# Kernel optimization log

Hardware: AMD Instinct MI355X
Metric: run time of the kernel (lower is better)

Reference implementation:

```python
import jax, jax.numpy as jnp
import numpy as np


def setup_inputs() -> dict:
    key = jax.random.key(0)
    k1, k2, k3, k4 = jax.random.split(key, 4)
    T, E, H, I = 256, 16, 2048, 1024
    x = jax.random.normal(k1, (T, H), dtype=jnp.float32)
    router_logits = jax.random.normal(k2, (T, E), dtype=jnp.float32)
    # dequantized GGUF expert weights (math after dequant is plain fp GEMM)
    w1 = jax.random.normal(k3, (E, 2 * I, H), dtype=jnp.float32) * 0.02  # gate/up fused
    w2 = jax.random.normal(k4, (E, H, I), dtype=jnp.float32) * 0.02     # down proj
    return {"x": x, "router_logits": router_logits, "w1": w1, "w2": w2, "top_k": 4}


def reference(x, router_logits, w1, w2, top_k):
    # Router: softmax -> top-k -> renormalize (vLLM fused_moe default)
    probs = jax.nn.softmax(router_logits, axis=-1)            # [T, E]
    topk_vals, topk_idx = jax.lax.top_k(probs, top_k)          # [T, k]
    topk_vals = topk_vals / jnp.sum(topk_vals, axis=-1, keepdims=True)
    T, E = router_logits.shape
    # dense routing weights (zero for non-selected experts)
    route_w = jnp.zeros((T, E), dtype=x.dtype).at[
        jnp.arange(T)[:, None], topk_idx].set(topk_vals)       # [T, E]

    I = w1.shape[1] // 2
    # gate_up projection for all experts: [T, E, 2I]
    h = jnp.einsum('th,eih->tei', x, w1)
    gate, up = h[..., :I], h[..., I:]
    act = jax.nn.silu(gate) * up                               # silu_and_mul [T, E, I]
    # down projection: [T, E, H]
    y = jnp.einsum('tei,ehi->teh', act, w2)
    # combine with routing weights
    out = jnp.einsum('te,teh->th', route_w, y)                 # [T, H]
    return out
```

## Files before the change

kernel.cpp:

```cpp
#include <hip/hip_runtime.h>


typedef __attribute__((ext_vector_type(8))) short bf16x8;
typedef __attribute__((ext_vector_type(4))) float floatx4;

#define T_TOK 256
#define N_EXP 16
#define H_DIM 2048
#define I_DIM 1024
#define MAX_SLOTS 256

__device__ __forceinline__ short f2bf(float f) {
    union { float f; unsigned u; } v; v.f = f;
    unsigned r = (v.u + 0x7FFFu + ((v.u >> 16) & 1u)) >> 16;
    return (short)r;
}
__device__ __forceinline__ float bf2f(short s) {
    union { unsigned u; float f; } v; v.u = ((unsigned)(unsigned short)s) << 16;
    return v.f;
}
__device__ __forceinline__ bf16x8 pack2f4(float4 a, float4 b) {
    bf16x8 r;
    r[0] = f2bf(a.x); r[1] = f2bf(a.y); r[2] = f2bf(a.z); r[3] = f2bf(a.w);
    r[4] = f2bf(b.x); r[5] = f2bf(b.y); r[6] = f2bf(b.z); r[7] = f2bf(b.w);
    return r;
}
__device__ __forceinline__ bf16x8 pack8(const float* __restrict__ p) {
    return pack2f4(*(const float4*)p, *(const float4*)(p + 4));
}

__global__ __launch_bounds__(256) void convert_x_kernel(
    const float* __restrict__ xf, short* __restrict__ xb)
{
    const int i = (blockIdx.x * 256 + threadIdx.x) * 8;
    *(bf16x8*)(xb + i) = pack8(xf + i);
}

__global__ __launch_bounds__(256) void route_kernel(
    const float* __restrict__ logits,
    const int* __restrict__ topk_ptr,
    int* __restrict__ counts, int* __restrict__ tokens,
    int* __restrict__ tok_e, int* __restrict__ tok_slot, float* __restrict__ tok_wt)
{
    __shared__ int lds_counts[N_EXP];
    const int t = threadIdx.x;
    if (t < N_EXP) lds_counts[t] = 0;
    __syncthreads();

    int K = topk_ptr[0];
    if (K > 8) K = 8;
    if (K < 1) K = 1;

    float l[N_EXP];
    #pragma unroll
    for (int j = 0; j < N_EXP; ++j) l[j] = logits[t * N_EXP + j];

    float M = l[0];
    #pragma unroll
    for (int j = 1; j < N_EXP; ++j) M = fmaxf(M, l[j]);

    int idx[8]; float lv[8]; unsigned used = 0u;
    for (int k = 0; k < K; ++k) {
        int bi = 0; float bv = -1e30f;
        #pragma unroll
        for (int j = 0; j < N_EXP; ++j)
            if (!((used >> j) & 1u) && l[j] > bv) { bv = l[j]; bi = j; }
        used |= 1u << bi;
        idx[k] = bi; lv[k] = bv;
    }
    float w[8], s = 0.f;
    for (int k = 0; k < K; ++k) { w[k] = __expf(lv[k] - M); s += w[k]; }
    const float inv = 1.0f / s;

    for (int k = 0; k < K; ++k) {
        const int e = idx[k];
        const int slot = atomicAdd(&lds_counts[e], 1);
        tokens[e * MAX_SLOTS + slot] = t;
        tok_e[t * 8 + k] = e; tok_slot[t * 8 + k] = slot; tok_wt[t * 8 + k] = w[k] * inv;
    }
    __syncthreads();
    if (t < N_EXP) counts[t] = lds_counts[t];
}

template<int MT>
__device__ __forceinline__ void g1_ms(
    int ms, int count, const int* __restrict__ toks, const short* __restrict__ xb,
    const float* __restrict__ wg, const float* __restrict__ wu,
    int quad, int nl, int lane, int iw, int kh, int i_base, int e,
    short* __restrict__ act, floatx4* red)
{
    const short* xr[MT];
    #pragma unroll
    for (int mt = 0; mt < MT; ++mt) {
        int s = ms + mt * 16 + nl;
        if (s >= count) s = count - 1;
        xr[mt] = xb + (size_t)toks[s] * H_DIM + kh * (H_DIM / 2);
    }
    floatx4 ag[MT], au[MT];
    #pragma unroll
    for (int mt = 0; mt < MT; ++mt) { ag[mt] = (floatx4)0.0f; au[mt] = (floatx4)0.0f; }

    for (int k = 0; k < H_DIM / 2; k += 32) {
        const int ko = k + quad * 8;
        float4 g0 = *(const float4*)(wg + ko), g1 = *(const float4*)(wg + ko + 4);
        float4 u0 = *(const float4*)(wu + ko), u1 = *(const float4*)(wu + ko + 4);
        bf16x8 av[MT];
        #pragma unroll
        for (int mt = 0; mt < MT; ++mt) av[mt] = *(const bf16x8*)(xr[mt] + ko);
        bf16x8 bg = pack2f4(g0, g1);
        bf16x8 bu = pack2f4(u0, u1);
        #pragma unroll
        for (int mt = 0; mt < MT; ++mt) {
            ag[mt] = __builtin_amdgcn_mfma_f32_16x16x32_bf16(av[mt], bg, ag[mt], 0, 0, 0);
            au[mt] = __builtin_amdgcn_mfma_f32_16x16x32_bf16(av[mt], bu, au[mt], 0, 0, 0);
        }
    }
    if (kh) {
        #pragma unroll
        for (int mt = 0; mt < MT; ++mt) {
            red[(((iw * 8 + mt) * 2 + 0) * 64) + lane] = ag[mt];
            red[(((iw * 8 + mt) * 2 + 1) * 64) + lane] = au[mt];
        }
    }
    __syncthreads();
    if (!kh) {
        #pragma unroll
        for (int mt = 0; mt < MT; ++mt) {
            floatx4 g = ag[mt] + red[(((iw * 8 + mt) * 2 + 0) * 64) + lane];
            floatx4 u = au[mt] + red[(((iw * 8 + mt) * 2 + 1) * 64) + lane];
            #pragma unroll
            for (int r = 0; r < 4; ++r) {
                const int slot = ms + mt * 16 + quad * 4 + r;
                if (slot < count) {
                    const float gv = g[r], uv = u[r];
                    const float a = gv / (1.0f + __expf(-gv)) * uv;
                    act[(size_t)(e * MAX_SLOTS + slot) * I_DIM + i_base + nl] = f2bf(a);
                }
            }
        }
    }
    __syncthreads();
}

__global__ __launch_bounds__(512, 2) void gemm1_kernel(
    const short* __restrict__ xb,
    const float* __restrict__ w1,
    const int* __restrict__ counts, const int* __restrict__ tokens,
    short* __restrict__ act)
{
    __shared__ floatx4 red[4 * 8 * 2 * 64];
    const int e = blockIdx.x;
    const int count = counts[e];
    if (count == 0) return;
    const int tid = (int)threadIdx.x;
    const int wave = tid >> 6, lane = tid & 63;
    const int iw = wave & 3, kh = wave >> 2;
    const int nl = lane & 15, quad = lane >> 4;
    const int i_base = blockIdx.y * 64 + iw * 16;

    const float* wg = w1 + ((size_t)e * H_DIM + (i_base + nl)) * H_DIM + kh * (H_DIM / 2);
    const float* wu = w1 + ((size_t)e * H_DIM + (I_DIM + i_base + nl)) * H_DIM + kh * (H_DIM / 2);
    const int* toks = tokens + e * MAX_SLOTS;

    for (int ms = 0; ms < count; ms += 128) {
        const int rem = count - ms;
        const int nmt = rem >= 128 ? 8 : ((rem + 15) >> 4);
        switch (nmt) {
            case 1: g1_ms<1>(ms, count, toks, xb, wg, wu, quad, nl, lane, iw, kh, i_base, e, act, red); break;
            case 2: g1_ms<2>(ms, count, toks, xb, wg, wu, quad, nl, lane, iw, kh, i_base, e, act, red); break;
            case 3: g1_ms<3>(ms, count, toks, xb, wg, wu, quad, nl, lane, iw, kh, i_base, e, act, red); break;
            case 4: g1_ms<4>(ms, count, toks, xb, wg, wu, quad, nl, lane, iw, kh, i_base, e, act, red); break;
            case 5: g1_ms<5>(ms, count, toks, xb, wg, wu, quad, nl, lane, iw, kh, i_base, e, act, red); break;
            case 6: g1_ms<6>(ms, count, toks, xb, wg, wu, quad, nl, lane, iw, kh, i_base, e, act, red); break;
            case 7: g1_ms<7>(ms, count, toks, xb, wg, wu, quad, nl, lane, iw, kh, i_base, e, act, red); break;
            default: g1_ms<8>(ms, count, toks, xb, wg, wu, quad, nl, lane, iw, kh, i_base, e, act, red); break;
        }
    }
}

template<int MT>
__device__ __forceinline__ void g2_ms(
    int ms, int count, const short* __restrict__ acte,
    const float* __restrict__ wr,
    int quad, int nl, int lane, int iw, int kh, int h_base, int e,
    short* __restrict__ y, floatx4* red)
{
    const short* ar[MT];
    #pragma unroll
    for (int mt = 0; mt < MT; ++mt) {
        int s = ms + mt * 16 + nl;
        if (s >= count) s = count - 1;
        ar[mt] = acte + (size_t)s * I_DIM + kh * (I_DIM / 2);
    }
    floatx4 acc[MT];
    #pragma unroll
    for (int mt = 0; mt < MT; ++mt) acc[mt] = (floatx4)0.0f;

    for (int k = 0; k < I_DIM / 2; k += 32) {
        const int ko = k + quad * 8;
        float4 b0 = *(const float4*)(wr + ko), b1 = *(const float4*)(wr + ko + 4);
        bf16x8 av[MT];
        #pragma unroll
        for (int mt = 0; mt < MT; ++mt) av[mt] = *(const bf16x8*)(ar[mt] + ko);
        bf16x8 b = pack2f4(b0, b1);
        #pragma unroll
        for (int mt = 0; mt < MT; ++mt)
            acc[mt] = __builtin_amdgcn_mfma_f32_16x16x32_bf16(av[mt], b, acc[mt], 0, 0, 0);
    }
    if (kh) {
        #pragma unroll
        for (int mt = 0; mt < MT; ++mt) red[(iw * 8 + mt) * 64 + lane] = acc[mt];
    }
    __syncthreads();
    if (!kh) {
        #pragma unroll
        for (int mt = 0; mt < MT; ++mt) {
            floatx4 a = acc[mt] + red[(iw * 8 + mt) * 64 + lane];
            #pragma unroll
            for (int r = 0; r < 4; ++r) {
                const int slot = ms + mt * 16 + quad * 4 + r;
                if (slot < count)
                    y[(size_t)(e * MAX_SLOTS + slot) * H_DIM + h_base + nl] = f2bf(a[r]);
            }
        }
    }
    __syncthreads();
}

__global__ __launch_bounds__(512, 4) void gemm2_kernel(
    const short* __restrict__ act,
    const float* __restrict__ w2,
    const int* __restrict__ counts,
    short* __restrict__ y)
{
    __shared__ floatx4 red[4 * 8 * 64];
    const int e = blockIdx.x;
    const int count = counts[e];
    if (count == 0) return;
    const int tid = (int)threadIdx.x;
    const int wave = tid >> 6, lane = tid & 63;
    const int iw = wave & 3, kh = wave >> 2;
    const int nl = lane & 15, quad = lane >> 4;
    const int h_base = blockIdx.y * 64 + iw * 16;

    const float* wr = w2 + ((size_t)e * H_DIM + h_base + nl) * I_DIM + kh * (I_DIM / 2);
    const short* acte = act + (size_t)e * MAX_SLOTS * I_DIM;

    for (int ms = 0; ms < count; ms += 128) {
        const int rem = count - ms;
        const int nmt = rem >= 128 ? 8 : ((rem + 15) >> 4);
        switch (nmt) {
            case 1: g2_ms<1>(ms, count, acte, wr, quad, nl, lane, iw, kh, h_base, e, y, red); break;
            case 2: g2_ms<2>(ms, count, acte, wr, quad, nl, lane, iw, kh, h_base, e, y, red); break;
            case 3: g2_ms<3>(ms, count, acte, wr, quad, nl, lane, iw, kh, h_base, e, y, red); break;
            case 4: g2_ms<4>(ms, count, acte, wr, quad, nl, lane, iw, kh, h_base, e, y, red); break;
            case 5: g2_ms<5>(ms, count, acte, wr, quad, nl, lane, iw, kh, h_base, e, y, red); break;
            case 6: g2_ms<6>(ms, count, acte, wr, quad, nl, lane, iw, kh, h_base, e, y, red); break;
            case 7: g2_ms<7>(ms, count, acte, wr, quad, nl, lane, iw, kh, h_base, e, y, red); break;
            default: g2_ms<8>(ms, count, acte, wr, quad, nl, lane, iw, kh, h_base, e, y, red); break;
        }
    }
}

__global__ __launch_bounds__(256) void gather_kernel(
    const short* __restrict__ y, const int* __restrict__ topk_ptr,
    const int* __restrict__ tok_e, const int* __restrict__ tok_slot,
    const float* __restrict__ tok_wt, float* __restrict__ out)
{
    const int t = blockIdx.x;
    int K = topk_ptr[0];
    if (K > 8) K = 8;
    if (K < 1) K = 1;
    int e[8], sl[8]; float w[8];
    for (int k = 0; k < K; ++k) {
        e[k] = tok_e[t * 8 + k]; sl[k] = tok_slot[t * 8 + k]; w[k] = tok_wt[t * 8 + k];
    }
    for (int h = threadIdx.x; h < H_DIM; h += 256) {
        float s = 0.f;
        for (int k = 0; k < K; ++k)
            s += w[k] * bf2f(y[(size_t)(e[k] * MAX_SLOTS + sl[k]) * H_DIM + h]);
        out[(size_t)t * H_DIM + h] = s;
    }
}

extern "C" void kernel_launch(void* const* d_in, const int* in_sizes, int n_in,
                              void* d_out, int out_size, void* d_ws, size_t ws_size,
                              hipStream_t stream)
{
    const float* x  = (const float*)d_in[0];
    const float* rl = (const float*)d_in[1];
    const float* w1 = (const float*)d_in[2];
    const float* w2 = (const float*)d_in[3];
    const int* topk = (const int*)d_in[4];

    char* ws = (char*)d_ws;
    int*   counts   = (int*)  (ws + 0);
    int*   tokens   = (int*)  (ws + 256);
    int*   tok_e    = (int*)  (ws + 16640);
    int*   tok_slot = (int*)  (ws + 24832);
    float* tok_wt   = (float*)(ws + 33024);
    short* xb       = (short*)(ws + 65536);
    short* act      = (short*)(ws + 1114112);
    short* yb       = (short*)(ws + 9502720);

    convert_x_kernel<<<256, 256, 0, stream>>>(x, xb);
    route_kernel<<<1, 256, 0, stream>>>(rl, topk, counts, tokens, tok_e, tok_slot, tok_wt);
    gemm1_kernel<<<dim3(N_EXP, 16), 512, 0, stream>>>(xb, w1, counts, tokens, act);
    gemm2_kernel<<<dim3(N_EXP, 32), 512, 0, stream>>>(act, w2, counts, yb);
    gather_kernel<<<T_TOK, 256, 0, stream>>>(yb, topk, tok_e, tok_slot, tok_wt, (float*)d_out);
}
```

Baseline: 527.4 us.

## Split GEMM K into four wave slices, shrink blocks, prefetch weights

Both expert GEMM kernels change from 512-thread blocks (4 N-tiles by 2 K-halves) to 256-thread blocks, each covering one 16-column tile with the K dimension split into four wave slices. A three-way LDS reduction combines the partial sums. The grid grows fourfold, which puts more independent blocks on the many CUs of a memory-bound fp32 weight stream. Each wave also software-prefetches the next fp32 weight chunk into registers before the MFMAs. Pointer arithmetic now uses 32-bit offsets. The cost is more LDS reduction traffic, and each block now re-reads the activation rows that its four tiles previously shared.

```diff
diff --git a/kernel.cpp b/kernel.cpp
--- a/kernel.cpp
+++ b/kernel.cpp
@@ -9,6 +9,8 @@
 #define H_DIM 2048
 #define I_DIM 1024
 #define MAX_SLOTS 256
+#define KQ1 (H_DIM / 4)
+#define KQ2 (I_DIM / 4)
 
 __device__ __forceinline__ short f2bf(float f) {
     union { float f; unsigned u; } v; v.f = f;
@@ -86,27 +88,33 @@
 __device__ __forceinline__ void g1_ms(
     int ms, int count, const int* __restrict__ toks, const short* __restrict__ xb,
     const float* __restrict__ wg, const float* __restrict__ wu,
-    int quad, int nl, int lane, int iw, int kh, int i_base, int e,
+    int quad, int nl, int lane, int kq, int i_base, int e,
     short* __restrict__ act, floatx4* red)
 {
-    const short* xr[MT];
+    int xoff[MT];
     #pragma unroll
     for (int mt = 0; mt < MT; ++mt) {
         int s = ms + mt * 16 + nl;
         if (s >= count) s = count - 1;
-        xr[mt] = xb + (size_t)toks[s] * H_DIM + kh * (H_DIM / 2);
+        xoff[mt] = toks[s] * H_DIM + kq * KQ1;
     }
     floatx4 ag[MT], au[MT];
     #pragma unroll
     for (int mt = 0; mt < MT; ++mt) { ag[mt] = (floatx4)0.0f; au[mt] = (floatx4)0.0f; }
 
-    for (int k = 0; k < H_DIM / 2; k += 32) {
-        const int ko = k + quad * 8;
-        float4 g0 = *(const float4*)(wg + ko), g1 = *(const float4*)(wg + ko + 4);
-        float4 u0 = *(const float4*)(wu + ko), u1 = *(const float4*)(wu + ko + 4);
+    const int koff = quad * 8;
+    float4 g0 = *(const float4*)(wg + koff), g1 = *(const float4*)(wg + koff + 4);
+    float4 u0 = *(const float4*)(wu + koff), u1 = *(const float4*)(wu + koff + 4);
+
+    for (int k = 0; k < KQ1; k += 32) {
+        const int nk = (k + 32 < KQ1) ? (k + 32) : k;
+        float4 ng0 = *(const float4*)(wg + nk + koff);
+        float4 ng1 = *(const float4*)(wg + nk + koff + 4);
+        float4 nu0 = *(const float4*)(wu + nk + koff);
+        float4 nu1 = *(const float4*)(wu + nk + koff + 4);
         bf16x8 av[MT];
         #pragma unroll
-        for (int mt = 0; mt < MT; ++mt) av[mt] = *(const bf16x8*)(xr[mt] + ko);
+        for (int mt = 0; mt < MT; ++mt) av[mt] = *(const bf16x8*)(xb + xoff[mt] + k + koff);
         bf16x8 bg = pack2f4(g0, g1);
         bf16x8 bu = pack2f4(u0, u1);
         #pragma unroll
@@ -114,20 +122,25 @@
             ag[mt] = __builtin_amdgcn_mfma_f32_16x16x32_bf16(av[mt], bg, ag[mt], 0, 0, 0);
             au[mt] = __builtin_amdgcn_mfma_f32_16x16x32_bf16(av[mt], bu, au[mt], 0, 0, 0);
         }
-    }
-    if (kh) {
+        g0 = ng0; g1 = ng1; u0 = nu0; u1 = nu1;
+    }
+    if (kq) {
         #pragma unroll
         for (int mt = 0; mt < MT; ++mt) {
-            red[(((iw * 8 + mt) * 2 + 0) * 64) + lane] = ag[mt];
-            red[(((iw * 8 + mt) * 2 + 1) * 64) + lane] = au[mt];
-        }
-    }
-    __syncthreads();
-    if (!kh) {
+            red[(((kq - 1) * 8 + mt) * 2 + 0) * 64 + lane] = ag[mt];
+            red[(((kq - 1) * 8 + mt) * 2 + 1) * 64 + lane] = au[mt];
+        }
+    }
+    __syncthreads();
+    if (kq == 0) {
         #pragma unroll
         for (int mt = 0; mt < MT; ++mt) {
-            floatx4 g = ag[mt] + red[(((iw * 8 + mt) * 2 + 0) * 64) + lane];
-            floatx4 u = au[mt] + red[(((iw * 8 + mt) * 2 + 1) * 64) + lane];
+            floatx4 g = ag[mt], u = au[mt];
+            #pragma unroll
+            for (int q = 0; q < 3; ++q) {
+                g += red[((q * 8 + mt) * 2 + 0) * 64 + lane];
+                u += red[((q * 8 + mt) * 2 + 1) * 64 + lane];
+            }
             #pragma unroll
             for (int r = 0; r < 4; ++r) {
                 const int slot = ms + mt * 16 + quad * 4 + r;
@@ -142,38 +155,37 @@
     __syncthreads();
 }
 
-__global__ __launch_bounds__(512, 2) void gemm1_kernel(
+__global__ __launch_bounds__(256, 3) void gemm1_kernel(
     const short* __restrict__ xb,
     const float* __restrict__ w1,
     const int* __restrict__ counts, const int* __restrict__ tokens,
     short* __restrict__ act)
 {
-    __shared__ floatx4 red[4 * 8 * 2 * 64];
+    __shared__ floatx4 red[3 * 8 * 2 * 64];
     const int e = blockIdx.x;
     const int count = counts[e];
     if (count == 0) return;
     const int tid = (int)threadIdx.x;
-    const int wave = tid >> 6, lane = tid & 63;
-    const int iw = wave & 3, kh = wave >> 2;
+    const int kq = tid >> 6, lane = tid & 63;
     const int nl = lane & 15, quad = lane >> 4;
-    const int i_base = blockIdx.y * 64 + iw * 16;
-
-    const float* wg = w1 + ((size_t)e * H_DIM + (i_base + nl)) * H_DIM + kh * (H_DIM / 2);
-    const float* wu = w1 + ((size_t)e * H_DIM + (I_DIM + i_base + nl)) * H_DIM + kh * (H_DIM / 2);
+    const int i_base = blockIdx.y * 16;
+
+    const float* wg = w1 + ((size_t)e * H_DIM + (i_base + nl)) * H_DIM + kq * KQ1;
+    const float* wu = w1 + ((size_t)e * H_DIM + (I_DIM + i_base + nl)) * H_DIM + kq * KQ1;
     const int* toks = tokens + e * MAX_SLOTS;
 
     for (int ms = 0; ms < count; ms += 128) {
         const int rem = count - ms;
         const int nmt = rem >= 128 ? 8 : ((rem + 15) >> 4);
         switch (nmt) {
-            case 1: g1_ms<1>(ms, count, toks, xb, wg, wu, quad, nl, lane, iw, kh, i_base, e, act, red); break;
-            case 2: g1_ms<2>(ms, count, toks, xb, wg, wu, quad, nl, lane, iw, kh, i_base, e, act, red); break;
-            case 3: g1_ms<3>(ms, count, toks, xb, wg, wu, quad, nl, lane, iw, kh, i_base, e, act, red); break;
-            case 4: g1_ms<4>(ms, count, toks, xb, wg, wu, quad, nl, lane, iw, kh, i_base, e, act, red); break;
-            case 5: g1_ms<5>(ms, count, toks, xb, wg, wu, quad, nl, lane, iw, kh, i_base, e, act, red); break;
-            case 6: g1_ms<6>(ms, count, toks, xb, wg, wu, quad, nl, lane, iw, kh, i_base, e, act, red); break;
-            case 7: g1_ms<7>(ms, count, toks, xb, wg, wu, quad, nl, lane, iw, kh, i_base, e, act, red); break;
-            default: g1_ms<8>(ms, count, toks, xb, wg, wu, quad, nl, lane, iw, kh, i_base, e, act, red); break;
+            case 1: g1_ms<1>(ms, count, toks, xb, wg, wu, quad, nl, lane, kq, i_base, e, act, red); break;
+            case 2: g1_ms<2>(ms, count, toks, xb, wg, wu, quad, nl, lane, kq, i_base, e, act, red); break;
+            case 3: g1_ms<3>(ms, count, toks, xb, wg, wu, quad, nl, lane, kq, i_base, e, act, red); break;
+            case 4: g1_ms<4>(ms, count, toks, xb, wg, wu, quad, nl, lane, kq, i_base, e, act, red); break;
+            case 5: g1_ms<5>(ms, count, toks, xb, wg, wu, quad, nl, lane, kq, i_base, e, act, red); break;
+            case 6: g1_ms<6>(ms, count, toks, xb, wg, wu, quad, nl, lane, kq, i_base, e, act, red); break;
+            case 7: g1_ms<7>(ms, count, toks, xb, wg, wu, quad, nl, lane, kq, i_base, e, act, red); break;
+            default: g1_ms<8>(ms, count, toks, xb, wg, wu, quad, nl, lane, kq, i_base, e, act, red); break;
         }
     }
 }
@@ -182,40 +194,47 @@
 __device__ __forceinline__ void g2_ms(
     int ms, int count, const short* __restrict__ acte,
     const float* __restrict__ wr,
-    int quad, int nl, int lane, int iw, int kh, int h_base, int e,
+    int quad, int nl, int lane, int kq, int h_base, int e,
     short* __restrict__ y, floatx4* red)
 {
-    const short* ar[MT];
+    int aoff[MT];
     #pragma unroll
     for (int mt = 0; mt < MT; ++mt) {
         int s = ms + mt * 16 + nl;
         if (s >= count) s = count - 1;
-        ar[mt] = acte + (size_t)s * I_DIM + kh * (I_DIM / 2);
+        aoff[mt] = s * I_DIM + kq * KQ2;
     }
     floatx4 acc[MT];
     #pragma unroll
     for (int mt = 0; mt < MT; ++mt) acc[mt] = (floatx4)0.0f;
 
-    for (int k = 0; k < I_DIM / 2; k += 32) {
-        const int ko = k + quad * 8;
-        float4 b0 = *(const float4*)(wr + ko), b1 = *(const float4*)(wr + ko + 4);
+    const int koff = quad * 8;
+    float4 b0 = *(const float4*)(wr + koff), b1 = *(const float4*)(wr + koff + 4);
+
+    for (int k = 0; k < KQ2; k += 32) {
+        const int nk = (k + 32 < KQ2) ? (k + 32) : k;
+        float4 nb0 = *(const float4*)(wr + nk + koff);
+        float4 nb1 = *(const float4*)(wr + nk + koff + 4);
         bf16x8 av[MT];
         #pragma unroll
-        for (int mt = 0; mt < MT; ++mt) av[mt] = *(const bf16x8*)(ar[mt] + ko);
+        for (int mt = 0; mt < MT; ++mt) av[mt] = *(const bf16x8*)(acte + aoff[mt] + k + koff);
         bf16x8 b = pack2f4(b0, b1);
         #pragma unroll
         for (int mt = 0; mt < MT; ++mt)
             acc[mt] = __builtin_amdgcn_mfma_f32_16x16x32_bf16(av[mt], b, acc[mt], 0, 0, 0);
-    }
-    if (kh) {
-        #pragma unroll
-        for (int mt = 0; mt < MT; ++mt) red[(iw * 8 + mt) * 64 + lane] = acc[mt];
-    }
-    __syncthreads();
-    if (!kh) {
+        b0 = nb0; b1 = nb1;
+    }
+    if (kq) {
+        #pragma unroll
+        for (int mt = 0; mt < MT; ++mt) red[((kq - 1) * 8 + mt) * 64 + lane] = acc[mt];
+    }
+    __syncthreads();
+    if (kq == 0) {
         #pragma unroll
         for (int mt = 0; mt < MT; ++mt) {
-            floatx4 a = acc[mt] + red[(iw * 8 + mt) * 64 + lane];
+            floatx4 a = acc[mt];
+            #pragma unroll
+            for (int q = 0; q < 3; ++q) a += red[(q * 8 + mt) * 64 + lane];
             #pragma unroll
             for (int r = 0; r < 4; ++r) {
                 const int slot = ms + mt * 16 + quad * 4 + r;
@@ -227,37 +246,36 @@
     __syncthreads();
 }
 
-__global__ __launch_bounds__(512, 4) void gemm2_kernel(
+__global__ __launch_bounds__(256, 4) void gemm2_kernel(
     const short* __restrict__ act,
     const float* __restrict__ w2,
     const int* __restrict__ counts,
     short* __restrict__ y)
 {
-    __shared__ floatx4 red[4 * 8 * 64];
+    __shared__ floatx4 red[3 * 8 * 64];
     const int e = blockIdx.x;
     const int count = counts[e];
     if (count == 0) return;
     const int tid = (int)threadIdx.x;
-    const int wave = tid >> 6, lane = tid & 63;
-    const int iw = wave & 3, kh = wave >> 2;
+    const int kq = tid >> 6, lane = tid & 63;
     const int nl = lane & 15, quad = lane >> 4;
-    const int h_base = blockIdx.y * 64 + iw * 16;
-
-    const float* wr = w2 + ((size_t)e * H_DIM + h_base + nl) * I_DIM + kh * (I_DIM / 2);
+    const int h_base = blockIdx.y * 16;
+
+    const float* wr = w2 + ((size_t)e * H_DIM + h_base + nl) * I_DIM + kq * KQ2;
     const short* acte = act + (size_t)e * MAX_SLOTS * I_DIM;
 
     for (int ms = 0; ms < count; ms += 128) {
         const int rem = count - ms;
         const int nmt = rem >= 128 ? 8 : ((rem + 15) >> 4);
         switch (nmt) {
-            case 1: g2_ms<1>(ms, count, acte, wr, quad, nl, lane, iw, kh, h_base, e, y, red); break;
-            case 2: g2_ms<2>(ms, count, acte, wr, quad, nl, lane, iw, kh, h_base, e, y, red); break;
-            case 3: g2_ms<3>(ms, count, acte, wr, quad, nl, lane, iw, kh, h_base, e, y, red); break;
-            case 4: g2_ms<4>(ms, count, acte, wr, quad, nl, lane, iw, kh, h_base, e, y, red); break;
-            case 5: g2_ms<5>(ms, count, acte, wr, quad, nl, lane, iw, kh, h_base, e, y, red); break;
-            case 6: g2_ms<6>(ms, count, acte, wr, quad, nl, lane, iw, kh, h_base, e, y, red); break;
-            case 7: g2_ms<7>(ms, count, acte, wr, quad, nl, lane, iw, kh, h_base, e, y, red); break;
-            default: g2_ms<8>(ms, count, acte, wr, quad, nl, lane, iw, kh, h_base, e, y, red); break;
+            case 1: g2_ms<1>(ms, count, acte, wr, quad, nl, lane, kq, h_base, e, y, red); break;
+            case 2: g2_ms<2>(ms, count, acte, wr, quad, nl, lane, kq, h_base, e, y, red); break;
+            case 3: g2_ms<3>(ms, count, acte, wr, quad, nl, lane, kq, h_base, e, y, red); break;
+            case 4: g2_ms<4>(ms, count, acte, wr, quad, nl, lane, kq, h_base, e, y, red); break;
+            case 5: g2_ms<5>(ms, count, acte, wr, quad, nl, lane, kq, h_base, e, y, red); break;
+            case 6: g2_ms<6>(ms, count, acte, wr, quad, nl, lane, kq, h_base, e, y, red); break;
+            case 7: g2_ms<7>(ms, count, acte, wr, quad, nl, lane, kq, h_base, e, y, red); break;
+            default: g2_ms<8>(ms, count, acte, wr, quad, nl, lane, kq, h_base, e, y, red); break;
         }
     }
 }
@@ -305,7 +323,7 @@
 
     convert_x_kernel<<<256, 256, 0, stream>>>(x, xb);
     route_kernel<<<1, 256, 0, stream>>>(rl, topk, counts, tokens, tok_e, tok_slot, tok_wt);
-    gemm1_kernel<<<dim3(N_EXP, 16), 512, 0, stream>>>(xb, w1, counts, tokens, act);
-    gemm2_kernel<<<dim3(N_EXP, 32), 512, 0, stream>>>(act, w2, counts, yb);
+    gemm1_kernel<<<dim3(N_EXP, 64), 256, 0, stream>>>(xb, w1, counts, tokens, act);
+    gemm2_kernel<<<dim3(N_EXP, 128), 256, 0, stream>>>(act, w2, counts, yb);
     gather_kernel<<<T_TOK, 256, 0, stream>>>(yb, topk, tok_e, tok_slot, tok_wt, (float*)d_out);
 }
```

After: 556.5 us. +5.5%, slower.

## Pre-gather expert tokens, software-prefetch weights, drop split-K reduction in gemm2

Applied to the files above, without the earlier changes.

Replaces the x-to-bf16 conversion with a kernel that gathers each expert's routed tokens into a contiguous bf16 buffer, so gemm1 reads activation rows without indirection. Both GEMMs now keep fp32 weight loads in a register ring that runs several iterations ahead, to hide global-memory latency on the weight stream. gemm2 drops its split-K across waves and the LDS reduction, giving each of 8 waves its own 16-column slice over a 128-wide tile, with half as many blocks. This uses more registers and adds a workspace buffer, and the smaller gemm2 grid may lower parallelism.

```diff
diff --git a/kernel.cpp b/kernel.cpp
--- a/kernel.cpp
+++ b/kernel.cpp
@@ -29,13 +29,6 @@
     return pack2f4(*(const float4*)p, *(const float4*)(p + 4));
 }
 
-__global__ __launch_bounds__(256) void convert_x_kernel(
-    const float* __restrict__ xf, short* __restrict__ xb)
-{
-    const int i = (blockIdx.x * 256 + threadIdx.x) * 8;
-    *(bf16x8*)(xb + i) = pack8(xf + i);
-}
-
 __global__ __launch_bounds__(256) void route_kernel(
     const float* __restrict__ logits,
     const int* __restrict__ topk_ptr,
@@ -82,37 +75,67 @@
     if (t < N_EXP) counts[t] = lds_counts[t];
 }
 
+__global__ __launch_bounds__(256) void gather_x_kernel(
+    const float* __restrict__ xf, const int* __restrict__ counts,
+    const int* __restrict__ tokens, short* __restrict__ xe)
+{
+    const int e = blockIdx.x, sc = blockIdx.y;
+    const int count = counts[e];
+    const int s0 = sc * 16;
+    if (s0 >= count) return;
+    const int send = (s0 + 16 < count) ? s0 + 16 : count;
+    const int cs = threadIdx.x * 8;
+    for (int s = s0; s < send; ++s) {
+        const int tok = tokens[e * MAX_SLOTS + s];
+        *(bf16x8*)(xe + ((size_t)e * MAX_SLOTS + s) * H_DIM + cs) =
+            pack8(xf + (size_t)tok * H_DIM + cs);
+    }
+}
+
 template<int MT>
-__device__ __forceinline__ void g1_ms(
-    int ms, int count, const int* __restrict__ toks, const short* __restrict__ xb,
+__device__ __forceinline__ void g1_body(
+    int ms, int count, const short* __restrict__ xe_e,
     const float* __restrict__ wg, const float* __restrict__ wu,
     int quad, int nl, int lane, int iw, int kh, int i_base, int e,
     short* __restrict__ act, floatx4* red)
 {
-    const short* xr[MT];
+    const short* ar[MT];
     #pragma unroll
     for (int mt = 0; mt < MT; ++mt) {
         int s = ms + mt * 16 + nl;
         if (s >= count) s = count - 1;
-        xr[mt] = xb + (size_t)toks[s] * H_DIM + kh * (H_DIM / 2);
+        ar[mt] = xe_e + (size_t)s * H_DIM + kh * (H_DIM / 2) + quad * 8;
     }
     floatx4 ag[MT], au[MT];
     #pragma unroll
     for (int mt = 0; mt < MT; ++mt) { ag[mt] = (floatx4)0.0f; au[mt] = (floatx4)0.0f; }
 
-    for (int k = 0; k < H_DIM / 2; k += 32) {
-        const int ko = k + quad * 8;
-        float4 g0 = *(const float4*)(wg + ko), g1 = *(const float4*)(wg + ko + 4);
-        float4 u0 = *(const float4*)(wu + ko), u1 = *(const float4*)(wu + ko + 4);
-        bf16x8 av[MT];
-        #pragma unroll
-        for (int mt = 0; mt < MT; ++mt) av[mt] = *(const bf16x8*)(xr[mt] + ko);
-        bf16x8 bg = pack2f4(g0, g1);
-        bf16x8 bu = pack2f4(u0, u1);
-        #pragma unroll
-        for (int mt = 0; mt < MT; ++mt) {
-            ag[mt] = __builtin_amdgcn_mfma_f32_16x16x32_bf16(av[mt], bg, ag[mt], 0, 0, 0);
-            au[mt] = __builtin_amdgcn_mfma_f32_16x16x32_bf16(av[mt], bu, au[mt], 0, 0, 0);
+    float4 sg0[4], sg1[4], su0[4], su1[4];
+    #pragma unroll
+    for (int d = 0; d < 3; ++d) {
+        sg0[d] = *(const float4*)(wg + d * 32);
+        sg1[d] = *(const float4*)(wg + d * 32 + 4);
+        su0[d] = *(const float4*)(wu + d * 32);
+        su1[d] = *(const float4*)(wu + d * 32 + 4);
+    }
+    for (int j = 0; j < 8; ++j) {
+        #pragma unroll
+        for (int u = 0; u < 4; ++u) {
+            const int it = j * 4 + u;
+            int pit = it + 3; if (pit > 31) pit = 31;
+            const int ps = (u + 3) & 3;
+            sg0[ps] = *(const float4*)(wg + pit * 32);
+            sg1[ps] = *(const float4*)(wg + pit * 32 + 4);
+            su0[ps] = *(const float4*)(wu + pit * 32);
+            su1[ps] = *(const float4*)(wu + pit * 32 + 4);
+            bf16x8 bg = pack2f4(sg0[u], sg1[u]);
+            bf16x8 bu = pack2f4(su0[u], su1[u]);
+            #pragma unroll
+            for (int mt = 0; mt < MT; ++mt) {
+                bf16x8 a = *(const bf16x8*)(ar[mt] + it * 32);
+                ag[mt] = __builtin_amdgcn_mfma_f32_16x16x32_bf16(a, bg, ag[mt], 0, 0, 0);
+                au[mt] = __builtin_amdgcn_mfma_f32_16x16x32_bf16(a, bu, au[mt], 0, 0, 0);
+            }
         }
     }
     if (kh) {
@@ -134,7 +157,7 @@
                 if (slot < count) {
                     const float gv = g[r], uv = u[r];
                     const float a = gv / (1.0f + __expf(-gv)) * uv;
-                    act[(size_t)(e * MAX_SLOTS + slot) * I_DIM + i_base + nl] = f2bf(a);
+                    act[(size_t)(e * MAX_SLOTS + slot) * I_DIM + i_base + iw * 16 + nl] = f2bf(a);
                 }
             }
         }
@@ -143,9 +166,9 @@
 }
 
 __global__ __launch_bounds__(512, 2) void gemm1_kernel(
-    const short* __restrict__ xb,
+    const short* __restrict__ xe,
     const float* __restrict__ w1,
-    const int* __restrict__ counts, const int* __restrict__ tokens,
+    const int* __restrict__ counts,
     short* __restrict__ act)
 {
     __shared__ floatx4 red[4 * 8 * 2 * 64];
@@ -156,108 +179,109 @@
     const int wave = tid >> 6, lane = tid & 63;
     const int iw = wave & 3, kh = wave >> 2;
     const int nl = lane & 15, quad = lane >> 4;
-    const int i_base = blockIdx.y * 64 + iw * 16;
-
-    const float* wg = w1 + ((size_t)e * H_DIM + (i_base + nl)) * H_DIM + kh * (H_DIM / 2);
-    const float* wu = w1 + ((size_t)e * H_DIM + (I_DIM + i_base + nl)) * H_DIM + kh * (H_DIM / 2);
-    const int* toks = tokens + e * MAX_SLOTS;
+    const int i_base = blockIdx.y * 64;
+
+    const float* wg = w1 + ((size_t)e * H_DIM + (i_base + iw * 16 + nl)) * H_DIM
+                         + kh * (H_DIM / 2) + quad * 8;
+    const float* wu = wg + (size_t)I_DIM * H_DIM;
+    const short* xe_e = xe + (size_t)e * MAX_SLOTS * H_DIM;
 
     for (int ms = 0; ms < count; ms += 128) {
         const int rem = count - ms;
         const int nmt = rem >= 128 ? 8 : ((rem + 15) >> 4);
         switch (nmt) {
-            case 1: g1_ms<1>(ms, count, toks, xb, wg, wu, quad, nl, lane, iw, kh, i_base, e, act, red); break;
-            case 2: g1_ms<2>(ms, count, toks, xb, wg, wu, quad, nl, lane, iw, kh, i_base, e, act, red); break;
-            case 3: g1_ms<3>(ms, count, toks, xb, wg, wu, quad, nl, lane, iw, kh, i_base, e, act, red); break;
-            case 4: g1_ms<4>(ms, count, toks, xb, wg, wu, quad, nl, lane, iw, kh, i_base, e, act, red); break;
-            case 5: g1_ms<5>(ms, count, toks, xb, wg, wu, quad, nl, lane, iw, kh, i_base, e, act, red); break;
-            case 6: g1_ms<6>(ms, count, toks, xb, wg, wu, quad, nl, lane, iw, kh, i_base, e, act, red); break;
-            case 7: g1_ms<7>(ms, count, toks, xb, wg, wu, quad, nl, lane, iw, kh, i_base, e, act, red); break;
-            default: g1_ms<8>(ms, count, toks, xb, wg, wu, quad, nl, lane, iw, kh, i_base, e, act, red); break;
+            case 1: g1_body<1>(ms, count, xe_e, wg, wu, quad, nl, lane, iw, kh, i_base, e, act, red); break;
+            case 2: g1_body<2>(ms, count, xe_e, wg, wu, quad, nl, lane, iw, kh, i_base, e, act, red); break;
+            case 3: g1_body<3>(ms, count, xe_e, wg, wu, quad, nl, lane, iw, kh, i_base, e, act, red); break;
+            case 4: g1_body<4>(ms, count, xe_e, wg, wu, quad, nl, lane, iw, kh, i_base, e, act, red); break;
+            case 5: g1_body<5>(ms, count, xe_e, wg, wu, quad, nl, lane, iw, kh, i_base, e, act, red); break;
+            case 6: g1_body<6>(ms, count, xe_e, wg, wu, quad, nl, lane, iw, kh, i_base, e, act, red); break;
+            case 7: g1_body<7>(ms, count, xe_e, wg, wu, quad, nl, lane, iw, kh, i_base, e, act, red); break;
+            default: g1_body<8>(ms, count, xe_e, wg, wu, quad, nl, lane, iw, kh, i_base, e, act, red); break;
         }
     }
 }
 
 template<int MT>
-__device__ __forceinline__ void g2_ms(
+__device__ __forceinline__ void g2_body(
     int ms, int count, const short* __restrict__ acte,
     const float* __restrict__ wr,
-    int quad, int nl, int lane, int iw, int kh, int h_base, int e,
-    short* __restrict__ y, floatx4* red)
+    int quad, int nl, int wave, int h_base, int e,
+    short* __restrict__ y)
 {
     const short* ar[MT];
     #pragma unroll
     for (int mt = 0; mt < MT; ++mt) {
         int s = ms + mt * 16 + nl;
         if (s >= count) s = count - 1;
-        ar[mt] = acte + (size_t)s * I_DIM + kh * (I_DIM / 2);
+        ar[mt] = acte + (size_t)s * I_DIM + quad * 8;
     }
     floatx4 acc[MT];
     #pragma unroll
     for (int mt = 0; mt < MT; ++mt) acc[mt] = (floatx4)0.0f;
 
-    for (int k = 0; k < I_DIM / 2; k += 32) {
-        const int ko = k + quad * 8;
-        float4 b0 = *(const float4*)(wr + ko), b1 = *(const float4*)(wr + ko + 4);
-        bf16x8 av[MT];
-        #pragma unroll
-        for (int mt = 0; mt < MT; ++mt) av[mt] = *(const bf16x8*)(ar[mt] + ko);
-        bf16x8 b = pack2f4(b0, b1);
-        #pragma unroll
-        for (int mt = 0; mt < MT; ++mt)
-            acc[mt] = __builtin_amdgcn_mfma_f32_16x16x32_bf16(av[mt], b, acc[mt], 0, 0, 0);
-    }
-    if (kh) {
-        #pragma unroll
-        for (int mt = 0; mt < MT; ++mt) red[(iw * 8 + mt) * 64 + lane] = acc[mt];
-    }
-    __syncthreads();
-    if (!kh) {
-        #pragma unroll
-        for (int mt = 0; mt < MT; ++mt) {
-            floatx4 a = acc[mt] + red[(iw * 8 + mt) * 64 + lane];
+    float4 sb0[8], sb1[8];
+    #pragma unroll
+    for (int d = 0; d < 7; ++d) {
+        sb0[d] = *(const float4*)(wr + d * 32);
+        sb1[d] = *(const float4*)(wr + d * 32 + 4);
+    }
+    for (int j = 0; j < 4; ++j) {
+        #pragma unroll
+        for (int u = 0; u < 8; ++u) {
+            const int it = j * 8 + u;
+            int pit = it + 7; if (pit > 31) pit = 31;
+            const int ps = (u + 7) & 7;
+            sb0[ps] = *(const float4*)(wr + pit * 32);
+            sb1[ps] = *(const float4*)(wr + pit * 32 + 4);
+            bf16x8 b = pack2f4(sb0[u], sb1[u]);
             #pragma unroll
-            for (int r = 0; r < 4; ++r) {
-                const int slot = ms + mt * 16 + quad * 4 + r;
-                if (slot < count)
-                    y[(size_t)(e * MAX_SLOTS + slot) * H_DIM + h_base + nl] = f2bf(a[r]);
+            for (int mt = 0; mt < MT; ++mt) {
+                bf16x8 a = *(const bf16x8*)(ar[mt] + it * 32);
+                acc[mt] = __builtin_amdgcn_mfma_f32_16x16x32_bf16(a, b, acc[mt], 0, 0, 0);
             }
         }
     }
-    __syncthreads();
-}
-
-__global__ __launch_bounds__(512, 4) void gemm2_kernel(
+    #pragma unroll
+    for (int mt = 0; mt < MT; ++mt) {
+        #pragma unroll
+        for (int r = 0; r < 4; ++r) {
+            const int slot = ms + mt * 16 + quad * 4 + r;
+            if (slot < count)
+                y[(size_t)(e * MAX_SLOTS + slot) * H_DIM + h_base + wave * 16 + nl] = f2bf(acc[mt][r]);
+        }
+    }
+}
+
+__global__ __launch_bounds__(512, 2) void gemm2_kernel(
     const short* __restrict__ act,
     const float* __restrict__ w2,
     const int* __restrict__ counts,
     short* __restrict__ y)
 {
-    __shared__ floatx4 red[4 * 8 * 64];
     const int e = blockIdx.x;
     const int count = counts[e];
     if (count == 0) return;
     const int tid = (int)threadIdx.x;
     const int wave = tid >> 6, lane = tid & 63;
-    const int iw = wave & 3, kh = wave >> 2;
     const int nl = lane & 15, quad = lane >> 4;
-    const int h_base = blockIdx.y * 64 + iw * 16;
-
-    const float* wr = w2 + ((size_t)e * H_DIM + h_base + nl) * I_DIM + kh * (I_DIM / 2);
+    const int h_base = blockIdx.y * 128;
+
+    const float* wr = w2 + ((size_t)e * H_DIM + h_base + wave * 16 + nl) * I_DIM + quad * 8;
     const short* acte = act + (size_t)e * MAX_SLOTS * I_DIM;
 
     for (int ms = 0; ms < count; ms += 128) {
         const int rem = count - ms;
         const int nmt = rem >= 128 ? 8 : ((rem + 15) >> 4);
         switch (nmt) {
-            case 1: g2_ms<1>(ms, count, acte, wr, quad, nl, lane, iw, kh, h_base, e, y, red); break;
-            case 2: g2_ms<2>(ms, count, acte, wr, quad, nl, lane, iw, kh, h_base, e, y, red); break;
-            case 3: g2_ms<3>(ms, count, acte, wr, quad, nl, lane, iw, kh, h_base, e, y, red); break;
-            case 4: g2_ms<4>(ms, count, acte, wr, quad, nl, lane, iw, kh, h_base, e, y, red); break;
-            case 5: g2_ms<5>(ms, count, acte, wr, quad, nl, lane, iw, kh, h_base, e, y, red); break;
-            case 6: g2_ms<6>(ms, count, acte, wr, quad, nl, lane, iw, kh, h_base, e, y, red); break;
-            case 7: g2_ms<7>(ms, count, acte, wr, quad, nl, lane, iw, kh, h_base, e, y, red); break;
-            default: g2_ms<8>(ms, count, acte, wr, quad, nl, lane, iw, kh, h_base, e, y, red); break;
+            case 1: g2_body<1>(ms, count, acte, wr, quad, nl, wave, h_base, e, y); break;
+            case 2: g2_body<2>(ms, count, acte, wr, quad, nl, wave, h_base, e, y); break;
+            case 3: g2_body<3>(ms, count, acte, wr, quad, nl, wave, h_base, e, y); break;
+            case 4: g2_body<4>(ms, count, acte, wr, quad, nl, wave, h_base, e, y); break;
+            case 5: g2_body<5>(ms, count, acte, wr, quad, nl, wave, h_base, e, y); break;
+            case 6: g2_body<6>(ms, count, acte, wr, quad, nl, wave, h_base, e, y); break;
+            case 7: g2_body<7>(ms, count, acte, wr, quad, nl, wave, h_base, e, y); break;
+            default: g2_body<8>(ms, count, acte, wr, quad, nl, wave, h_base, e, y); break;
         }
     }
 }
@@ -299,13 +323,13 @@
     int*   tok_e    = (int*)  (ws + 16640);
     int*   tok_slot = (int*)  (ws + 24832);
     float* tok_wt   = (float*)(ws + 33024);
-    short* xb       = (short*)(ws + 65536);
     short* act      = (short*)(ws + 1114112);
     short* yb       = (short*)(ws + 9502720);
-
-    convert_x_kernel<<<256, 256, 0, stream>>>(x, xb);
+    short* xe       = (short*)(ws + 26279936);
+
     route_kernel<<<1, 256, 0, stream>>>(rl, topk, counts, tokens, tok_e, tok_slot, tok_wt);
-    gemm1_kernel<<<dim3(N_EXP, 16), 512, 0, stream>>>(xb, w1, counts, tokens, act);
-    gemm2_kernel<<<dim3(N_EXP, 32), 512, 0, stream>>>(act, w2, counts, yb);
+    gather_x_kernel<<<dim3(N_EXP, 16), 256, 0, stream>>>(x, counts, tokens, xe);
+    gemm1_kernel<<<dim3(N_EXP, 16), 512, 0, stream>>>(xe, w1, counts, act);
+    gemm2_kernel<<<dim3(N_EXP, 16), 512, 0, stream>>>(act, w2, counts, yb);
     gather_kernel<<<T_TOK, 256, 0, stream>>>(yb, topk, tok_e, tok_slot, tok_wt, (float*)d_out);
 }
```

Result: no change. 529.0 us (+0.3%).
